# Performance work log

Hardware: AMD Instinct MI355X
Metric: run time of the kernel (lower is better)

## Reference

```python
import jax, jax.numpy as jnp
import numpy as np
import math


def _dct2_mat(N):
    # DCT-II matrix, norm=None convention of torch_dct: X[k] = 2*sum_n x[n]*cos(pi*(2n+1)*k/(2N))
    n = np.arange(N)
    k = n[:, None]
    C = 2.0 * np.cos(np.pi * (2 * n[None, :] + 1) * k / (2 * N))
    return jnp.asarray(C, dtype=jnp.float32)


def setup_inputs() -> dict:
    key = jax.random.key(0)
    k1, k2, k3 = jax.random.split(key, 3)
    B, H, W = 128, 256, 256
    thresh = int(H / (2 * math.sqrt(2)))  # 90
    x = jax.random.normal(k1, (B, 3, H, W), dtype=jnp.float32)
    w = jax.random.normal(k2, (1, thresh), dtype=jnp.float32) * 0.05
    b = jax.random.normal(k3, (1,), dtype=jnp.float32) * 0.05
    return {"x": x, "w": w, "b": b}


def reference(x, w, b):
    B, C, H, W = x.shape
    Ch = _dct2_mat(H)
    Cw = _dct2_mat(W)
    # dct_2d: DCT-II along last two dims
    xd = jnp.einsum('bchw,kw->bchk', x, Cw)
    xd = jnp.einsum('bchk,jh->bcjk', xd, Ch)
    xd = jax.lax.stop_gradient(xd)  # original does x.detach() inside get_fft_feature
    gray = 0.2989 * xd[:, 0] + 0.587 * xd[:, 1] + 0.114 * xd[:, 2]  # [B,H,W]
    F = jnp.fft.fft2(gray, axes=(-2, -1))
    re = F.real + 1e-8  # original adds epsilon to both real and imag parts
    im = F.imag + 1e-8
    mag = jnp.log(jnp.sqrt(re * re + im * im + 1e-10) + 1e-10)
    mag = jnp.fft.fftshift(mag, axes=(-2, -1))  # quadrant-swap `shift` == fftshift for even dims
    # radial binning (static integer radii, as in azimuthalAverage)
    yy, xx = np.indices([H, W])
    r = np.sqrt((xx - H / 2) ** 2 + (yy - W / 2) ** 2).astype(np.int32).ravel()
    nbins = int(r.max()) + 1
    nr = jnp.asarray(np.bincount(r, minlength=nbins).astype(np.float32))
    rj = jnp.asarray(r)
    tbin = jax.vmap(lambda m: jax.ops.segment_sum(m, rj, num_segments=nbins))(mag.reshape(B, -1))
    prof = tbin / (nr + 1e-10)  # [B, nbins]
    prof = prof[:, 1:-2]  # azimuthalAverage returns radial_prof[1:-2]
    mn = jnp.min(prof, axis=1, keepdims=True)
    mx = jnp.max(prof, axis=1, keepdims=True)
    out = (prof - mn) / (mx - mn)
    out = jnp.where(jnp.isnan(out), 0.0, out)
    thresh = w.shape[1]
    feat = out[:, -thresh:]  # [B, thresh]
    return feat @ w.T + b  # [B, 1]
```

## Files before the change

### kernel.cpp

```cpp
#include <hip/hip_runtime.h>
#include <math.h>

#define NBINS 182
#define NB 128

typedef unsigned short u16;
typedef __attribute__((ext_vector_type(8))) short short8;
typedef __attribute__((ext_vector_type(4))) float f32x4;

__device__ __forceinline__ u16 f2bf(float f) {
    union { float f; unsigned u; } v; v.f = f;
    unsigned r = v.u + 0x7FFF + ((v.u >> 16) & 1);
    return (u16)(r >> 16);
}
__device__ __forceinline__ float bf2f(u16 u) {
    union { unsigned u; float f; } v; v.u = ((unsigned)u) << 16;
    return v.f;
}
__device__ __forceinline__ short8 negbf(short8 v) {
    short8 r;
#pragma unroll
    for (int i = 0; i < 8; ++i) r[i] = v[i] ^ (short)0x8000;
    return r;
}

__device__ __forceinline__ int radial_bin(int dx, int dy) {
    int d2 = dx * dx + dy * dy;
    int bin = (int)sqrtf((float)d2);
    while ((bin + 1) * (bin + 1) <= d2) ++bin;
    while (bin * bin > d2) --bin;
    return bin;
}

__global__ __launch_bounds__(256) void prep(const float* __restrict__ x,
                                            u16* __restrict__ G,
                                            float* __restrict__ M_re,
                                            float* __restrict__ M_im,
                                            u16* __restrict__ A1,
                                            float* __restrict__ nrpart,
                                            float* __restrict__ tbin,
                                            u16* __restrict__ Tt_im) {
    __shared__ double ctab[1024];
    __shared__ double stab[1024];
    __shared__ float s[NBINS];
    int blk = blockIdx.x;
    int t = threadIdx.x;

    if (blk < 256) {
        for (int i = t; i < 1024; i += 256) {
            double a = 3.14159265358979323846 * (double)i / 512.0;
            ctab[i] = cos(a);
            stab[i] = sin(a);
        }
        __syncthreads();
        int j = blk;
        int w = t;
        double re = 0.0, im = 0.0;
        int tw = 2 * w + 1;
        for (int k = 0; k < 256; ++k) {
            int e = (4 * j * k) & 1023;
            int m = (tw * k) & 1023;
            double cw = 2.0 * ctab[m];
            re += ctab[e] * cw;
            im -= stab[e] * cw;
        }
        M_re[j * 256 + w] = (float)re;
        M_im[j * 256 + w] = (float)im;
        A1[j * 256 + w] = f2bf((float)re);
        A1[(j + 256) * 256 + w] = f2bf((float)im);
    } else if (blk < 512) {
        int i = blk - 256;
        if (t < NBINS) s[t] = 0.0f;
        __syncthreads();
        int bin = radial_bin(t - 128, i - 128);
        atomicAdd(&s[bin], 1.0f);
        __syncthreads();
        if (t < NBINS) nrpart[i * NBINS + t] = s[t];
    } else if (blk < 544) {
        int idx = (blk - 512) * 256 + t;
        for (int i = idx; i < NB * NBINS; i += 32 * 256) tbin[i] = 0.0f;
        for (int i = idx; i < NB * 128; i += 32 * 256) {
            int b = i >> 7, off = (i & 127) << 1;
            *(unsigned*)(Tt_im + (size_t)b * 65536 + 128 * 256 + off) = 0u;
        }
    } else {
        int tid = (blk - 544) * 256 + t;
        for (int i = tid; i < 2097152; i += 262144) {
            int idx = i * 4;
            int b = idx >> 16;
            int rem = idx & 65535;
            const float* p = x + (size_t)b * 196608 + rem;
            float4 r = *(const float4*)p;
            float4 g = *(const float4*)(p + 65536);
            float4 bl = *(const float4*)(p + 131072);
            float g0 = 0.2989f * r.x + 0.587f * g.x + 0.114f * bl.x;
            float g1 = 0.2989f * r.y + 0.587f * g.y + 0.114f * bl.y;
            float g2 = 0.2989f * r.z + 0.587f * g.z + 0.114f * bl.z;
            float g3 = 0.2989f * r.w + 0.587f * g.w + 0.114f * bl.w;
            uint2 o;
            o.x = (unsigned)f2bf(g0) | ((unsigned)f2bf(g1) << 16);
            o.y = (unsigned)f2bf(g2) | ((unsigned)f2bf(g3) << 16);
            *(uint2*)(G + idx) = o;
        }
    }
}

__global__ __launch_bounds__(256) void s1(const u16* __restrict__ A1,
                                          const u16* __restrict__ G,
                                          u16* __restrict__ Tt_re,
                                          u16* __restrict__ Tt_im) {
    int b = blockIdx.z;
    int t = threadIdx.x;

    if (blockIdx.y == 2) {
        int lane = t & 63, wv = t >> 6;
        int fr = lane & 15;
        int fk = (lane >> 4) << 3;
        const u16* Ap = A1 + (size_t)(128 + fr) * 256;
        const u16* Gb = G + (size_t)b * 65536;
        int c0 = blockIdx.x * 128 + wv * 32;
        f32x4 acc[2];
        acc[0] = (f32x4){0.f, 0.f, 0.f, 0.f};
        acc[1] = (f32x4){0.f, 0.f, 0.f, 0.f};
        for (int kk = 0; kk < 256; kk += 32) {
            short8 af = *(const short8*)(Ap + kk + fk);
#pragma unroll
            for (int sub = 0; sub < 2; ++sub) {
                short8 bfv = *(const short8*)(Gb + (size_t)(c0 + sub * 16 + fr) * 256 + kk + fk);
                acc[sub] = __builtin_amdgcn_mfma_f32_16x16x32_bf16(
                    af, bfv, acc[sub], 0, 0, 0);
            }
        }
        if ((lane >> 4) == 0) {
            size_t base = (size_t)b * 65536 + 128 * 256;
            Tt_re[base + c0 + lane] = f2bf(acc[0][0]);
            Tt_re[base + c0 + 16 + lane] = f2bf(acc[1][0]);
        }
        return;
    }

    __shared__ u16 As[128 * 40];
    __shared__ u16 Bs[128 * 40];
    int r0 = blockIdx.y * 256;
    int h0 = blockIdx.x * 128;
    int lane = t & 63, wv = t >> 6;
    int wr = (wv >> 1) * 64;
    int wc = (wv & 1) * 64;
    int fr = lane & 15;
    int fk = (lane >> 4) << 3;

    f32x4 acc[4][4];
#pragma unroll
    for (int i = 0; i < 4; ++i)
#pragma unroll
        for (int j = 0; j < 4; ++j) acc[i][j] = (f32x4){0.f, 0.f, 0.f, 0.f};

    const u16* Ap = A1 + (size_t)r0 * 256;
    const u16* Gp = G + (size_t)b * 65536 + (size_t)h0 * 256;

    for (int kk = 0; kk < 256; kk += 32) {
#pragma unroll
        for (int c = t; c < 512; c += 256) {
            int row = c >> 2, off = (c & 3) << 3;
            *(uint4*)&As[row * 40 + off] =
                *(const uint4*)(Ap + (size_t)row * 256 + kk + off);
            *(uint4*)&Bs[row * 40 + off] =
                *(const uint4*)(Gp + (size_t)row * 256 + kk + off);
        }
        __syncthreads();
        short8 af[4], bfr[4];
#pragma unroll
        for (int i = 0; i < 4; ++i)
            af[i] = *(const short8*)&As[(wr + i * 16 + fr) * 40 + fk];
#pragma unroll
        for (int j = 0; j < 4; ++j)
            bfr[j] = *(const short8*)&Bs[(wc + j * 16 + fr) * 40 + fk];
#pragma unroll
        for (int i = 0; i < 4; ++i)
#pragma unroll
            for (int j = 0; j < 4; ++j)
                acc[i][j] = __builtin_amdgcn_mfma_f32_16x16x32_bf16(
                    af[i], bfr[j], acc[i][j], 0, 0, 0);
        __syncthreads();
    }

    u16* dst = ((r0 < 256) ? Tt_re : Tt_im) + (size_t)b * 65536;
    int rq = (lane >> 4) << 2;
#pragma unroll
    for (int i = 0; i < 4; ++i)
#pragma unroll
        for (int j = 0; j < 4; ++j) {
            int col = h0 + wc + j * 16 + fr;
#pragma unroll
            for (int reg = 0; reg < 4; ++reg) {
                int row = wr + i * 16 + rq + reg;
                dst[(size_t)row * 256 + col] = f2bf(acc[i][j][reg]);
            }
        }
}

__global__ __launch_bounds__(256) void s2f(const u16* __restrict__ A1,
                                           const float* __restrict__ M_re,
                                           const u16* __restrict__ Tt_re,
                                           const u16* __restrict__ Tt_im,
                                           float* __restrict__ tbin) {
    __shared__ u16 Ar[64 * 40], Ai[64 * 40], Br[64 * 40], Bi[64 * 40];
    __shared__ float sbins[NBINS];
    __shared__ float sM[256];
    int blk = blockIdx.x;
    int t = threadIdx.x;

    if (blk >= 1024) {
        int b = blk - 1024;
        sM[t] = M_re[128 * 256 + t];
        __syncthreads();
        if (t > 128) return;
        const u16* pr = Tt_re + (size_t)b * 65536 + (size_t)t * 256;
        const u16* pi = Tt_im + (size_t)b * 65536 + (size_t)t * 256;
        float re = 0.0f, im = 0.0f;
        for (int h = 0; h < 256; h += 8) {
            uint4 vr = *(const uint4*)(pr + h);
            uint4 vi = *(const uint4*)(pi + h);
            unsigned wr[4] = {vr.x, vr.y, vr.z, vr.w};
            unsigned wi[4] = {vi.x, vi.y, vi.z, vi.w};
#pragma unroll
            for (int q = 0; q < 4; ++q) {
                re = fmaf(sM[h + 2 * q], bf2f((u16)(wr[q] & 0xffff)), re);
                re = fmaf(sM[h + 2 * q + 1], bf2f((u16)(wr[q] >> 16)), re);
                im = fmaf(sM[h + 2 * q], bf2f((u16)(wi[q] & 0xffff)), im);
                im = fmaf(sM[h + 2 * q + 1], bf2f((u16)(wi[q] >> 16)), im);
            }
        }
        re += 1e-8f; im += 1e-8f;
        float mag = logf(sqrtf(re * re + im * im + 1e-10f) + 1e-10f);
        float wj = (t == 0 || t == 128) ? 1.0f : 2.0f;
        int dx = (t < 128) ? t : t - 256;
        int bin = radial_bin(dx, -128);
        atomicAdd(&tbin[b * NBINS + bin], wj * mag);
        return;
    }

    int b = blk >> 3;
    int u0 = ((blk >> 2) & 1) * 64;
    int j0 = (blk & 3) * 64;
    int lane = t & 63, wv = t >> 6;
    int wu = (wv >> 1) * 32;
    int wj = (wv & 1) * 32;
    int fr = lane & 15;
    int fk = (lane >> 4) << 3;

    for (int i = t; i < NBINS; i += 256) sbins[i] = 0.0f;

    f32x4 accr[2][2], acci[2][2];
#pragma unroll
    for (int i = 0; i < 2; ++i)
#pragma unroll
        for (int j = 0; j < 2; ++j) {
            accr[i][j] = (f32x4){0.f, 0.f, 0.f, 0.f};
            acci[i][j] = (f32x4){0.f, 0.f, 0.f, 0.f};
        }

    const u16* Apr = A1 + (size_t)u0 * 256;
    const u16* Api = A1 + (size_t)(256 + u0) * 256;

    int lrow = t >> 2, loff = (t & 3) << 3;
    int jp = j0 + lrow;
    int src = (jp <= 128) ? jp : 256 - jp;
    unsigned imask = (jp > 128) ? 0x80008000u : 0u;
    const u16* Trs = Tt_re + (size_t)b * 65536 + (size_t)src * 256;
    const u16* Tis = Tt_im + (size_t)b * 65536 + (size_t)src * 256;

    for (int kk = 0; kk < 256; kk += 32) {
        *(uint4*)&Ar[lrow * 40 + loff] =
            *(const uint4*)(Apr + (size_t)lrow * 256 + kk + loff);
        *(uint4*)&Ai[lrow * 40 + loff] =
            *(const uint4*)(Api + (size_t)lrow * 256 + kk + loff);
        *(uint4*)&Br[lrow * 40 + loff] = *(const uint4*)(Trs + kk + loff);
        uint4 vi = *(const uint4*)(Tis + kk + loff);
        vi.x ^= imask; vi.y ^= imask; vi.z ^= imask; vi.w ^= imask;
        *(uint4*)&Bi[lrow * 40 + loff] = vi;
        __syncthreads();
        short8 arf[2], aif[2], naif[2], brf[2], bif[2];
#pragma unroll
        for (int i = 0; i < 2; ++i) {
            arf[i] = *(const short8*)&Ar[(wu + i * 16 + fr) * 40 + fk];
            aif[i] = *(const short8*)&Ai[(wu + i * 16 + fr) * 40 + fk];
            naif[i] = negbf(aif[i]);
        }
#pragma unroll
        for (int j = 0; j < 2; ++j) {
            brf[j] = *(const short8*)&Br[(wj + j * 16 + fr) * 40 + fk];
            bif[j] = *(const short8*)&Bi[(wj + j * 16 + fr) * 40 + fk];
        }
#pragma unroll
        for (int i = 0; i < 2; ++i)
#pragma unroll
            for (int j = 0; j < 2; ++j) {
                accr[i][j] = __builtin_amdgcn_mfma_f32_16x16x32_bf16(
                    arf[i], brf[j], accr[i][j], 0, 0, 0);
                accr[i][j] = __builtin_amdgcn_mfma_f32_16x16x32_bf16(
                    naif[i], bif[j], accr[i][j], 0, 0, 0);
                acci[i][j] = __builtin_amdgcn_mfma_f32_16x16x32_bf16(
                    arf[i], bif[j], acci[i][j], 0, 0, 0);
                acci[i][j] = __builtin_amdgcn_mfma_f32_16x16x32_bf16(
                    aif[i], brf[j], acci[i][j], 0, 0, 0);
            }
        __syncthreads();
    }

    int rq = (lane >> 4) << 2;
#pragma unroll
    for (int i = 0; i < 2; ++i)
#pragma unroll
        for (int j = 0; j < 2; ++j) {
            int v = j0 + wj + j * 16 + fr;
            int dx = (v < 128) ? v : v - 256;
#pragma unroll
            for (int reg = 0; reg < 4; ++reg) {
                int u = u0 + wu + i * 16 + rq + reg;
                float wrow = (u == 0) ? 1.0f : 2.0f;
                int bin = radial_bin(dx, u);
                float re = accr[i][j][reg] + 1e-8f;
                float im = acci[i][j][reg] + 1e-8f;
                float mag = logf(sqrtf(re * re + im * im + 1e-10f) + 1e-10f);
                atomicAdd(&sbins[bin], wrow * mag);
            }
        }
    __syncthreads();
    for (int i = t; i < NBINS; i += 256)
        atomicAdd(&tbin[b * NBINS + i], sbins[i]);
}

__global__ __launch_bounds__(192) void finalize(const float* __restrict__ tbin,
                                                const float* __restrict__ nrpart,
                                                const float* __restrict__ w,
                                                const float* __restrict__ bias,
                                                float* __restrict__ out) {
    __shared__ float prof[NBINS];
    __shared__ float smn, smx, ssum;
    int b = blockIdx.x;
    int t = threadIdx.x;
    if (t < NBINS) {
        float nr = 0.0f;
        for (int i = 0; i < 256; ++i) nr += nrpart[i * NBINS + t];
        prof[t] = tbin[b * NBINS + t] / (nr + 1e-10f);
    }
    __syncthreads();
    if (t == 0) {
        float mn = prof[1], mx = prof[1];
        for (int i = 2; i <= 179; ++i) {
            float p = prof[i];
            mn = fminf(mn, p);
            mx = fmaxf(mx, p);
        }
        smn = mn; smx = mx; ssum = 0.0f;
    }
    __syncthreads();
    if (t < 90) {
        float denom = smx - smn;
        float v = (prof[90 + t] - smn) / denom;
        if (v != v) v = 0.0f;
        atomicAdd(&ssum, v * w[t]);
    }
    __syncthreads();
    if (t == 0) out[b] = ssum + bias[0];
}

extern "C" void kernel_launch(void* const* d_in, const int* in_sizes, int n_in,
                              void* d_out, int out_size, void* d_ws, size_t ws_size,
                              hipStream_t stream) {
    const float* x = (const float*)d_in[0];
    const float* w = (const float*)d_in[1];
    const float* bias = (const float*)d_in[2];
    float* out = (float*)d_out;

    float* M_re = (float*)d_ws;
    float* M_im = M_re + 65536;
    u16* A1 = (u16*)(M_im + 65536);
    u16* G = A1 + 131072;
    u16* Tt_re = G + (size_t)NB * 65536;
    u16* Tt_im = Tt_re + (size_t)NB * 65536;
    float* tbin = (float*)(Tt_im + (size_t)NB * 65536);
    float* nrpart = tbin + NB * NBINS;

    prep<<<1568, 256, 0, stream>>>(x, G, M_re, M_im, A1, nrpart, tbin, Tt_im);
    s1<<<dim3(2, 3, NB), 256, 0, stream>>>(A1, G, Tt_re, Tt_im);
    s2f<<<1152, 256, 0, stream>>>(A1, M_re, Tt_re, Tt_im, tbin);
    finalize<<<NB, 192, 0, stream>>>(tbin, nrpart, w, bias, out);
}
```

Baseline: 223.9 us.

## Exploit Hermitian symmetry in s2f to compute conjugate column pairs from shared fragments

The second FFT stage used to cover all 256 output columns by reading mirrored rows of the intermediate with sign flips. It now processes only columns 0..127 and builds the mirrored column 256-v from the same loaded fragments by recombining them with a negated imaginary B operand. Column 128 gets a separate small tile. This halves the s2f GEMM blocks and the B-tile loads, but each block issues twice the MFMAs into extra accumulators, which raises register pressure.

```diff
diff --git a/kernel.cpp b/kernel.cpp
--- a/kernel.cpp
+++ b/kernel.cpp
@@ -80,8 +80,8 @@
         int idx = (blk - 512) * 256 + t;
         for (int i = idx; i < NB * NBINS; i += 32 * 256) tbin[i] = 0.0f;
         for (int i = idx; i < NB * 128; i += 32 * 256) {
-            int b = i >> 7, off = (i & 127) << 1;
-            *(unsigned*)(Tt_im + (size_t)b * 65536 + 128 * 256 + off) = 0u;
+            int bb = i >> 7, off = (i & 127) << 1;
+            *(unsigned*)(Tt_im + (size_t)bb * 65536 + 128 * 256 + off) = 0u;
         }
     } else {
         int tid = (blk - 544) * 256 + t;
@@ -205,13 +205,14 @@
                                            const u16* __restrict__ Tt_im,
                                            float* __restrict__ tbin) {
     __shared__ u16 Ar[64 * 40], Ai[64 * 40], Br[64 * 40], Bi[64 * 40];
+    __shared__ u16 Br3[16 * 40], Bi3[16 * 40];
     __shared__ float sbins[NBINS];
     __shared__ float sM[256];
     int blk = blockIdx.x;
     int t = threadIdx.x;
 
-    if (blk >= 1024) {
-        int b = blk - 1024;
+    if (blk >= 512) {
+        int b = blk - 512;
         sM[t] = M_re[128 * 256 + t];
         __syncthreads();
         if (t > 128) return;
@@ -240,35 +241,42 @@
         return;
     }
 
-    int b = blk >> 3;
-    int u0 = ((blk >> 2) & 1) * 64;
-    int j0 = (blk & 3) * 64;
+    int b = blk >> 2;
+    int u0 = ((blk >> 1) & 1) * 64;
+    int j0 = (blk & 1) * 64;
     int lane = t & 63, wv = t >> 6;
     int wu = (wv >> 1) * 32;
     int wj = (wv & 1) * 32;
     int fr = lane & 15;
     int fk = (lane >> 4) << 3;
+    bool do128 = (j0 == 64) && ((wv & 1) == 0);
 
     for (int i = t; i < NBINS; i += 256) sbins[i] = 0.0f;
 
-    f32x4 accr[2][2], acci[2][2];
-#pragma unroll
-    for (int i = 0; i < 2; ++i)
+    f32x4 accr1[2][2], acci1[2][2], accr2[2][2], acci2[2][2];
+    f32x4 acc3r[2], acc3i[2];
+#pragma unroll
+    for (int i = 0; i < 2; ++i) {
 #pragma unroll
         for (int j = 0; j < 2; ++j) {
-            accr[i][j] = (f32x4){0.f, 0.f, 0.f, 0.f};
-            acci[i][j] = (f32x4){0.f, 0.f, 0.f, 0.f};
-        }
+            accr1[i][j] = (f32x4){0.f, 0.f, 0.f, 0.f};
+            acci1[i][j] = (f32x4){0.f, 0.f, 0.f, 0.f};
+            accr2[i][j] = (f32x4){0.f, 0.f, 0.f, 0.f};
+            acci2[i][j] = (f32x4){0.f, 0.f, 0.f, 0.f};
+        }
+        acc3r[i] = (f32x4){0.f, 0.f, 0.f, 0.f};
+        acc3i[i] = (f32x4){0.f, 0.f, 0.f, 0.f};
+    }
 
     const u16* Apr = A1 + (size_t)u0 * 256;
     const u16* Api = A1 + (size_t)(256 + u0) * 256;
 
     int lrow = t >> 2, loff = (t & 3) << 3;
-    int jp = j0 + lrow;
-    int src = (jp <= 128) ? jp : 256 - jp;
-    unsigned imask = (jp > 128) ? 0x80008000u : 0u;
-    const u16* Trs = Tt_re + (size_t)b * 65536 + (size_t)src * 256;
-    const u16* Tis = Tt_im + (size_t)b * 65536 + (size_t)src * 256;
+    const u16* Trs = Tt_re + (size_t)b * 65536 + (size_t)(j0 + lrow) * 256;
+    const u16* Tis = Tt_im + (size_t)b * 65536 + (size_t)(j0 + lrow) * 256;
+    int r3 = (t & 63) >> 2, o3 = (t & 3) << 3;
+    const u16* T3s = (((t >> 6) == 0) ? Tt_re : Tt_im)
+                   + (size_t)b * 65536 + (size_t)(128 + r3) * 256;
 
     for (int kk = 0; kk < 256; kk += 32) {
         *(uint4*)&Ar[lrow * 40 + loff] =
@@ -276,11 +284,14 @@
         *(uint4*)&Ai[lrow * 40 + loff] =
             *(const uint4*)(Api + (size_t)lrow * 256 + kk + loff);
         *(uint4*)&Br[lrow * 40 + loff] = *(const uint4*)(Trs + kk + loff);
-        uint4 vi = *(const uint4*)(Tis + kk + loff);
-        vi.x ^= imask; vi.y ^= imask; vi.z ^= imask; vi.w ^= imask;
-        *(uint4*)&Bi[lrow * 40 + loff] = vi;
-        __syncthreads();
-        short8 arf[2], aif[2], naif[2], brf[2], bif[2];
+        *(uint4*)&Bi[lrow * 40 + loff] = *(const uint4*)(Tis + kk + loff);
+        if (j0 == 64 && t < 128) {
+            uint4 v3 = *(const uint4*)(T3s + kk + o3);
+            if (t < 64) *(uint4*)&Br3[r3 * 40 + o3] = v3;
+            else        *(uint4*)&Bi3[r3 * 40 + o3] = v3;
+        }
+        __syncthreads();
+        short8 arf[2], aif[2], naif[2], brf[2], bif[2], nbif[2];
 #pragma unroll
         for (int i = 0; i < 2; ++i) {
             arf[i] = *(const short8*)&Ar[(wu + i * 16 + fr) * 40 + fk];
@@ -291,20 +302,44 @@
         for (int j = 0; j < 2; ++j) {
             brf[j] = *(const short8*)&Br[(wj + j * 16 + fr) * 40 + fk];
             bif[j] = *(const short8*)&Bi[(wj + j * 16 + fr) * 40 + fk];
+            nbif[j] = negbf(bif[j]);
         }
 #pragma unroll
         for (int i = 0; i < 2; ++i)
 #pragma unroll
             for (int j = 0; j < 2; ++j) {
-                accr[i][j] = __builtin_amdgcn_mfma_f32_16x16x32_bf16(
-                    arf[i], brf[j], accr[i][j], 0, 0, 0);
-                accr[i][j] = __builtin_amdgcn_mfma_f32_16x16x32_bf16(
-                    naif[i], bif[j], accr[i][j], 0, 0, 0);
-                acci[i][j] = __builtin_amdgcn_mfma_f32_16x16x32_bf16(
-                    arf[i], bif[j], acci[i][j], 0, 0, 0);
-                acci[i][j] = __builtin_amdgcn_mfma_f32_16x16x32_bf16(
-                    aif[i], brf[j], acci[i][j], 0, 0, 0);
-            }
+                accr1[i][j] = __builtin_amdgcn_mfma_f32_16x16x32_bf16(
+                    arf[i], brf[j], accr1[i][j], 0, 0, 0);
+                accr1[i][j] = __builtin_amdgcn_mfma_f32_16x16x32_bf16(
+                    naif[i], bif[j], accr1[i][j], 0, 0, 0);
+                acci1[i][j] = __builtin_amdgcn_mfma_f32_16x16x32_bf16(
+                    arf[i], bif[j], acci1[i][j], 0, 0, 0);
+                acci1[i][j] = __builtin_amdgcn_mfma_f32_16x16x32_bf16(
+                    aif[i], brf[j], acci1[i][j], 0, 0, 0);
+                accr2[i][j] = __builtin_amdgcn_mfma_f32_16x16x32_bf16(
+                    arf[i], brf[j], accr2[i][j], 0, 0, 0);
+                accr2[i][j] = __builtin_amdgcn_mfma_f32_16x16x32_bf16(
+                    aif[i], bif[j], accr2[i][j], 0, 0, 0);
+                acci2[i][j] = __builtin_amdgcn_mfma_f32_16x16x32_bf16(
+                    arf[i], nbif[j], acci2[i][j], 0, 0, 0);
+                acci2[i][j] = __builtin_amdgcn_mfma_f32_16x16x32_bf16(
+                    aif[i], brf[j], acci2[i][j], 0, 0, 0);
+            }
+        if (do128) {
+            short8 brf3 = *(const short8*)&Br3[fr * 40 + fk];
+            short8 bif3 = *(const short8*)&Bi3[fr * 40 + fk];
+#pragma unroll
+            for (int i = 0; i < 2; ++i) {
+                acc3r[i] = __builtin_amdgcn_mfma_f32_16x16x32_bf16(
+                    arf[i], brf3, acc3r[i], 0, 0, 0);
+                acc3r[i] = __builtin_amdgcn_mfma_f32_16x16x32_bf16(
+                    naif[i], bif3, acc3r[i], 0, 0, 0);
+                acc3i[i] = __builtin_amdgcn_mfma_f32_16x16x32_bf16(
+                    arf[i], bif3, acc3i[i], 0, 0, 0);
+                acc3i[i] = __builtin_amdgcn_mfma_f32_16x16x32_bf16(
+                    aif[i], brf3, acc3i[i], 0, 0, 0);
+            }
+        }
         __syncthreads();
     }
 
@@ -314,18 +349,40 @@
 #pragma unroll
         for (int j = 0; j < 2; ++j) {
             int v = j0 + wj + j * 16 + fr;
-            int dx = (v < 128) ? v : v - 256;
 #pragma unroll
             for (int reg = 0; reg < 4; ++reg) {
                 int u = u0 + wu + i * 16 + rq + reg;
                 float wrow = (u == 0) ? 1.0f : 2.0f;
-                int bin = radial_bin(dx, u);
-                float re = accr[i][j][reg] + 1e-8f;
-                float im = acci[i][j][reg] + 1e-8f;
+                float re1 = accr1[i][j][reg] + 1e-8f;
+                float im1 = acci1[i][j][reg] + 1e-8f;
+                float m1 = logf(sqrtf(re1 * re1 + im1 * im1 + 1e-10f) + 1e-10f);
+                float val;
+                if (v == 0) {
+                    val = wrow * m1;
+                } else {
+                    float re2 = accr2[i][j][reg] + 1e-8f;
+                    float im2 = acci2[i][j][reg] + 1e-8f;
+                    float m2 = logf(sqrtf(re2 * re2 + im2 * im2 + 1e-10f) + 1e-10f);
+                    val = wrow * (m1 + m2);
+                }
+                int bin = radial_bin(v, u);
+                atomicAdd(&sbins[bin], val);
+            }
+        }
+    if (do128 && fr == 0) {
+#pragma unroll
+        for (int i = 0; i < 2; ++i)
+#pragma unroll
+            for (int reg = 0; reg < 4; ++reg) {
+                int u = u0 + wu + i * 16 + rq + reg;
+                float wrow = (u == 0) ? 1.0f : 2.0f;
+                float re = acc3r[i][reg] + 1e-8f;
+                float im = acc3i[i][reg] + 1e-8f;
                 float mag = logf(sqrtf(re * re + im * im + 1e-10f) + 1e-10f);
+                int bin = radial_bin(-128, u);
                 atomicAdd(&sbins[bin], wrow * mag);
             }
-        }
+    }
     __syncthreads();
     for (int i = t; i < NBINS; i += 256)
         atomicAdd(&tbin[b * NBINS + i], sbins[i]);
@@ -385,6 +442,6 @@
 
     prep<<<1568, 256, 0, stream>>>(x, G, M_re, M_im, A1, nrpart, tbin, Tt_im);
     s1<<<dim3(2, 3, NB), 256, 0, stream>>>(A1, G, Tt_re, Tt_im);
-    s2f<<<1152, 256, 0, stream>>>(A1, M_re, Tt_re, Tt_im, tbin);
+    s2f<<<640, 256, 0, stream>>>(A1, M_re, Tt_re, Tt_im, tbin);
     finalize<<<NB, 192, 0, stream>>>(tbin, nrpart, w, bias, out);
 }
```

Measured after the change: 208.5 us. 1.07x faster.

## Exploit conjugate symmetry in second-stage transform, computing v and -v together

Applied to the files above, without the earlier changes.

The second-stage complex GEMM is reworked to compute the positive and negative frequency columns (v and 256-v) from the same source rows in one pass, using the conjugate symmetry of the real-input spectrum. Each block now covers a whole row of u for 32 columns with 512 threads and reads fragments directly from global memory instead of staging through shared memory, which removes the LDS tiles and per-iteration barriers. The Nyquist column is handled by a separate extra MFMA path. The intent is to halve the operand loading and drop synchronisation, at the cost of more registers per thread, uncoalesced direct global fragment loads, and a small amount of wasted MFMA work on zero operands.

```diff
diff --git a/kernel.cpp b/kernel.cpp
--- a/kernel.cpp
+++ b/kernel.cpp
@@ -31,6 +31,8 @@
     while (bin * bin > d2) --bin;
     return bin;
 }
+
+#define MFMA __builtin_amdgcn_mfma_f32_16x16x32_bf16
 
 __global__ __launch_bounds__(256) void prep(const float* __restrict__ x,
                                             u16* __restrict__ G,
@@ -80,8 +82,8 @@
         int idx = (blk - 512) * 256 + t;
         for (int i = idx; i < NB * NBINS; i += 32 * 256) tbin[i] = 0.0f;
         for (int i = idx; i < NB * 128; i += 32 * 256) {
-            int b = i >> 7, off = (i & 127) << 1;
-            *(unsigned*)(Tt_im + (size_t)b * 65536 + 128 * 256 + off) = 0u;
+            int bb = i >> 7, off = (i & 127) << 1;
+            *(unsigned*)(Tt_im + (size_t)bb * 65536 + 128 * 256 + off) = 0u;
         }
     } else {
         int tid = (blk - 544) * 256 + t;
@@ -127,8 +129,7 @@
 #pragma unroll
             for (int sub = 0; sub < 2; ++sub) {
                 short8 bfv = *(const short8*)(Gb + (size_t)(c0 + sub * 16 + fr) * 256 + kk + fk);
-                acc[sub] = __builtin_amdgcn_mfma_f32_16x16x32_bf16(
-                    af, bfv, acc[sub], 0, 0, 0);
+                acc[sub] = MFMA(af, bfv, acc[sub], 0, 0, 0);
             }
         }
         if ((lane >> 4) == 0) {
@@ -179,8 +180,7 @@
         for (int i = 0; i < 4; ++i)
 #pragma unroll
             for (int j = 0; j < 4; ++j)
-                acc[i][j] = __builtin_amdgcn_mfma_f32_16x16x32_bf16(
-                    af[i], bfr[j], acc[i][j], 0, 0, 0);
+                acc[i][j] = MFMA(af[i], bfr[j], acc[i][j], 0, 0, 0);
         __syncthreads();
     }
 
@@ -199,20 +199,19 @@
         }
 }
 
-__global__ __launch_bounds__(256) void s2f(const u16* __restrict__ A1,
+__global__ __launch_bounds__(512) void s2g(const u16* __restrict__ A1,
                                            const float* __restrict__ M_re,
                                            const u16* __restrict__ Tt_re,
                                            const u16* __restrict__ Tt_im,
                                            float* __restrict__ tbin) {
-    __shared__ u16 Ar[64 * 40], Ai[64 * 40], Br[64 * 40], Bi[64 * 40];
     __shared__ float sbins[NBINS];
     __shared__ float sM[256];
     int blk = blockIdx.x;
     int t = threadIdx.x;
 
-    if (blk >= 1024) {
-        int b = blk - 1024;
-        sM[t] = M_re[128 * 256 + t];
+    if (blk >= 512) {
+        int b = blk - 512;
+        if (t < 256) sM[t] = M_re[128 * 256 + t];
         __syncthreads();
         if (t > 128) return;
         const u16* pr = Tt_re + (size_t)b * 65536 + (size_t)t * 256;
@@ -224,11 +223,11 @@
             unsigned wr[4] = {vr.x, vr.y, vr.z, vr.w};
             unsigned wi[4] = {vi.x, vi.y, vi.z, vi.w};
 #pragma unroll
-            for (int q = 0; q < 4; ++q) {
-                re = fmaf(sM[h + 2 * q], bf2f((u16)(wr[q] & 0xffff)), re);
-                re = fmaf(sM[h + 2 * q + 1], bf2f((u16)(wr[q] >> 16)), re);
-                im = fmaf(sM[h + 2 * q], bf2f((u16)(wi[q] & 0xffff)), im);
-                im = fmaf(sM[h + 2 * q + 1], bf2f((u16)(wi[q] >> 16)), im);
+            for (int qq = 0; qq < 4; ++qq) {
+                re = fmaf(sM[h + 2 * qq], bf2f((u16)(wr[qq] & 0xffff)), re);
+                re = fmaf(sM[h + 2 * qq + 1], bf2f((u16)(wr[qq] >> 16)), re);
+                im = fmaf(sM[h + 2 * qq], bf2f((u16)(wi[qq] & 0xffff)), im);
+                im = fmaf(sM[h + 2 * qq + 1], bf2f((u16)(wi[qq] >> 16)), im);
             }
         }
         re += 1e-8f; im += 1e-8f;
@@ -240,94 +239,97 @@
         return;
     }
 
-    int b = blk >> 3;
-    int u0 = ((blk >> 2) & 1) * 64;
-    int j0 = (blk & 3) * 64;
+    int b = blk >> 2, q = blk & 3;
     int lane = t & 63, wv = t >> 6;
-    int wu = (wv >> 1) * 32;
-    int wj = (wv & 1) * 32;
     int fr = lane & 15;
     int fk = (lane >> 4) << 3;
-
-    for (int i = t; i < NBINS; i += 256) sbins[i] = 0.0f;
-
-    f32x4 accr[2][2], acci[2][2];
-#pragma unroll
-    for (int i = 0; i < 2; ++i)
-#pragma unroll
-        for (int j = 0; j < 2; ++j) {
-            accr[i][j] = (f32x4){0.f, 0.f, 0.f, 0.f};
-            acci[i][j] = (f32x4){0.f, 0.f, 0.f, 0.f};
-        }
-
-    const u16* Apr = A1 + (size_t)u0 * 256;
-    const u16* Api = A1 + (size_t)(256 + u0) * 256;
-
-    int lrow = t >> 2, loff = (t & 3) << 3;
-    int jp = j0 + lrow;
-    int src = (jp <= 128) ? jp : 256 - jp;
-    unsigned imask = (jp > 128) ? 0x80008000u : 0u;
-    const u16* Trs = Tt_re + (size_t)b * 65536 + (size_t)src * 256;
-    const u16* Tis = Tt_im + (size_t)b * 65536 + (size_t)src * 256;
+    int rq = (lane >> 4) << 2;
+
+    for (int i = t; i < NBINS; i += 512) sbins[i] = 0.0f;
+    __syncthreads();
+
+    const u16* Aur = A1 + (size_t)(16 * wv + fr) * 256;
+    const u16* Aui = A1 + (size_t)(256 + 16 * wv + fr) * 256;
+    const u16* Tr0 = Tt_re + (size_t)b * 65536 + (size_t)(32 * q + fr) * 256;
+    const u16* Ti0 = Tt_im + (size_t)b * 65536 + (size_t)(32 * q + fr) * 256;
+    const u16* T28 = Tt_re + (size_t)b * 65536 + (size_t)128 * 256;
+
+    f32x4 r1[2], i1[2], r2[2], i2[2], c3r, c3i;
+#pragma unroll
+    for (int j = 0; j < 2; ++j) {
+        r1[j] = (f32x4){0.f, 0.f, 0.f, 0.f};
+        i1[j] = (f32x4){0.f, 0.f, 0.f, 0.f};
+        r2[j] = (f32x4){0.f, 0.f, 0.f, 0.f};
+        i2[j] = (f32x4){0.f, 0.f, 0.f, 0.f};
+    }
+    c3r = (f32x4){0.f, 0.f, 0.f, 0.f};
+    c3i = (f32x4){0.f, 0.f, 0.f, 0.f};
+    const short8 z8 = (short8){0, 0, 0, 0, 0, 0, 0, 0};
 
     for (int kk = 0; kk < 256; kk += 32) {
-        *(uint4*)&Ar[lrow * 40 + loff] =
-            *(const uint4*)(Apr + (size_t)lrow * 256 + kk + loff);
-        *(uint4*)&Ai[lrow * 40 + loff] =
-            *(const uint4*)(Api + (size_t)lrow * 256 + kk + loff);
-        *(uint4*)&Br[lrow * 40 + loff] = *(const uint4*)(Trs + kk + loff);
-        uint4 vi = *(const uint4*)(Tis + kk + loff);
-        vi.x ^= imask; vi.y ^= imask; vi.z ^= imask; vi.w ^= imask;
-        *(uint4*)&Bi[lrow * 40 + loff] = vi;
-        __syncthreads();
-        short8 arf[2], aif[2], naif[2], brf[2], bif[2];
-#pragma unroll
-        for (int i = 0; i < 2; ++i) {
-            arf[i] = *(const short8*)&Ar[(wu + i * 16 + fr) * 40 + fk];
-            aif[i] = *(const short8*)&Ai[(wu + i * 16 + fr) * 40 + fk];
-            naif[i] = negbf(aif[i]);
-        }
-#pragma unroll
-        for (int j = 0; j < 2; ++j) {
-            brf[j] = *(const short8*)&Br[(wj + j * 16 + fr) * 40 + fk];
-            bif[j] = *(const short8*)&Bi[(wj + j * 16 + fr) * 40 + fk];
-        }
-#pragma unroll
-        for (int i = 0; i < 2; ++i)
-#pragma unroll
-            for (int j = 0; j < 2; ++j) {
-                accr[i][j] = __builtin_amdgcn_mfma_f32_16x16x32_bf16(
-                    arf[i], brf[j], accr[i][j], 0, 0, 0);
-                accr[i][j] = __builtin_amdgcn_mfma_f32_16x16x32_bf16(
-                    naif[i], bif[j], accr[i][j], 0, 0, 0);
-                acci[i][j] = __builtin_amdgcn_mfma_f32_16x16x32_bf16(
-                    arf[i], bif[j], acci[i][j], 0, 0, 0);
-                acci[i][j] = __builtin_amdgcn_mfma_f32_16x16x32_bf16(
-                    aif[i], brf[j], acci[i][j], 0, 0, 0);
+        short8 arf = *(const short8*)(Aur + kk + fk);
+        short8 aif = *(const short8*)(Aui + kk + fk);
+        short8 naif = negbf(aif);
+        short8 brf3 = z8;
+        if (q == 0 && fr == 0) brf3 = *(const short8*)(T28 + kk + fk);
+#pragma unroll
+        for (int vt = 0; vt < 2; ++vt) {
+            short8 brf = *(const short8*)(Tr0 + (size_t)(16 * vt) * 256 + kk + fk);
+            short8 bifv = *(const short8*)(Ti0 + (size_t)(16 * vt) * 256 + kk + fk);
+            short8 nbif = negbf(bifv);
+            r1[vt] = MFMA(arf, brf, r1[vt], 0, 0, 0);
+            r1[vt] = MFMA(naif, bifv, r1[vt], 0, 0, 0);
+            i1[vt] = MFMA(arf, bifv, i1[vt], 0, 0, 0);
+            i1[vt] = MFMA(aif, brf, i1[vt], 0, 0, 0);
+            r2[vt] = MFMA(arf, brf, r2[vt], 0, 0, 0);
+            r2[vt] = MFMA(aif, bifv, r2[vt], 0, 0, 0);
+            i2[vt] = MFMA(arf, nbif, i2[vt], 0, 0, 0);
+            i2[vt] = MFMA(aif, brf, i2[vt], 0, 0, 0);
+        }
+        if (q == 0) {
+            c3r = MFMA(arf, brf3, c3r, 0, 0, 0);
+            c3r = MFMA(naif, z8, c3r, 0, 0, 0);
+            c3i = MFMA(arf, z8, c3i, 0, 0, 0);
+            c3i = MFMA(aif, brf3, c3i, 0, 0, 0);
+        }
+    }
+
+#pragma unroll
+    for (int vt = 0; vt < 2; ++vt) {
+        int v = 32 * q + 16 * vt + fr;
+#pragma unroll
+        for (int reg = 0; reg < 4; ++reg) {
+            int u = 16 * wv + rq + reg;
+            float wrow = (u == 0) ? 1.0f : 2.0f;
+            float re1 = r1[vt][reg] + 1e-8f;
+            float im1 = i1[vt][reg] + 1e-8f;
+            float m1 = logf(sqrtf(re1 * re1 + im1 * im1 + 1e-10f) + 1e-10f);
+            float val;
+            if (v == 0) {
+                val = wrow * m1;
+            } else {
+                float re2 = r2[vt][reg] + 1e-8f;
+                float im2 = i2[vt][reg] + 1e-8f;
+                float m2 = logf(sqrtf(re2 * re2 + im2 * im2 + 1e-10f) + 1e-10f);
+                val = wrow * (m1 + m2);
             }
-        __syncthreads();
-    }
-
-    int rq = (lane >> 4) << 2;
-#pragma unroll
-    for (int i = 0; i < 2; ++i)
-#pragma unroll
-        for (int j = 0; j < 2; ++j) {
-            int v = j0 + wj + j * 16 + fr;
-            int dx = (v < 128) ? v : v - 256;
-#pragma unroll
-            for (int reg = 0; reg < 4; ++reg) {
-                int u = u0 + wu + i * 16 + rq + reg;
-                float wrow = (u == 0) ? 1.0f : 2.0f;
-                int bin = radial_bin(dx, u);
-                float re = accr[i][j][reg] + 1e-8f;
-                float im = acci[i][j][reg] + 1e-8f;
-                float mag = logf(sqrtf(re * re + im * im + 1e-10f) + 1e-10f);
-                atomicAdd(&sbins[bin], wrow * mag);
-            }
-        }
-    __syncthreads();
-    for (int i = t; i < NBINS; i += 256)
+            atomicAdd(&sbins[radial_bin(v, u)], val);
+        }
+    }
+    if (q == 0 && fr == 0) {
+#pragma unroll
+        for (int reg = 0; reg < 4; ++reg) {
+            int u = 16 * wv + rq + reg;
+            float wrow = (u == 0) ? 1.0f : 2.0f;
+            float re = c3r[reg] + 1e-8f;
+            float im = c3i[reg] + 1e-8f;
+            float mag = logf(sqrtf(re * re + im * im + 1e-10f) + 1e-10f);
+            atomicAdd(&sbins[radial_bin(-128, u)], wrow * mag);
+        }
+    }
+
+    __syncthreads();
+    for (int i = t; i < NBINS; i += 512)
         atomicAdd(&tbin[b * NBINS + i], sbins[i]);
 }
 
@@ -385,6 +387,6 @@
 
     prep<<<1568, 256, 0, stream>>>(x, G, M_re, M_im, A1, nrpart, tbin, Tt_im);
     s1<<<dim3(2, 3, NB), 256, 0, stream>>>(A1, G, Tt_re, Tt_im);
-    s2f<<<1152, 256, 0, stream>>>(A1, M_re, Tt_re, Tt_im, tbin);
+    s2g<<<640, 512, 0, stream>>>(A1, M_re, Tt_re, Tt_im, tbin);
     finalize<<<NB, 192, 0, stream>>>(tbin, nrpart, w, bias, out);
 }
```

Result: faster. 213.4 us (-4.7%).
